# Kernel optimization log

Measured on AMD Instinct MI355X. Metric: run time of the kernel, lower is better.

Reference implementation:

```python
import jax, jax.numpy as jnp
import numpy as np
from jax import lax

M = 8192  # number of candidate detections
C = 80    # number of classes (COCO)
MIN_CONF = 0.25
MIN_IOU = 0.45
VALID_CLASS_IDS = jnp.array([2, 3, 5, 7], dtype=jnp.int32)  # COCO vehicles


def setup_inputs() -> dict:
    key = jax.random.key(0)
    k1, k2, k3, k4, k5, k6, k7 = jax.random.split(key, 7)
    # boxes stored as (y1, x1, y2, x2) in input-image pixel space, guaranteed y1<y2, x1<x2
    y1 = jax.random.uniform(k1, (1, M)) * 600.0
    x1 = jax.random.uniform(k2, (1, M)) * 600.0
    h = jax.random.uniform(k3, (1, M)) * 120.0 + 4.0
    w = jax.random.uniform(k4, (1, M)) * 120.0 + 4.0
    boxes_raw = jnp.stack([y1, x1, y1 + h, x1 + w], axis=-1).astype(jnp.float32)  # [1,M,4]
    scores = jax.random.uniform(k5, (1, C, M), dtype=jnp.float32)  # [1,C,M]
    cls = jax.random.randint(k6, (1, M), 0, C, dtype=jnp.int32)
    idx = jax.random.randint(k7, (1, M), 0, M, dtype=jnp.int32)
    indices = jnp.stack([jnp.zeros_like(cls), cls, idx], axis=-1)  # [1,M,3]: (batch, class_id, box_idx)
    return {"boxes_raw": boxes_raw, "scores": scores, "indices": indices, "out_h": 640, "out_w": 640}


def _pairwise_iou(b):
    # b: [M,4] (x1,y1,x2,y2)
    x1, y1, x2, y2 = b[:, 0], b[:, 1], b[:, 2], b[:, 3]
    area = jnp.maximum(x2 - x1, 0.0) * jnp.maximum(y2 - y1, 0.0)  # [M]
    ix1 = jnp.maximum(x1[:, None], x1[None, :])
    iy1 = jnp.maximum(y1[:, None], y1[None, :])
    ix2 = jnp.minimum(x2[:, None], x2[None, :])
    iy2 = jnp.minimum(y2[:, None], y2[None, :])
    inter = jnp.maximum(ix2 - ix1, 0.0) * jnp.maximum(iy2 - iy1, 0.0)  # [M,M]
    return inter / (area[:, None] + area[None, :] - inter + 1e-9)


def _postprocess(boxes_raw, scores, indices, out_h, out_w):
    idxs = indices[0, :, 2]       # predicted-positive box indices [M]
    class_ids = indices[0, :, 1]  # class ids [M]
    conf = scores[0, class_ids, idxs]  # irregular gather [M]
    b = boxes_raw[0, idxs]  # [M,4] (y1,x1,y2,x2)
    # swap to (x1,y1,x2,y2) as in the original column permutation
    boxes = jnp.stack([b[:, 1], b[:, 0], b[:, 3], b[:, 2]], axis=-1)
    bounds = jnp.array([out_w, out_h, out_w, out_h], dtype=boxes.dtype)
    boxes = jnp.clip(boxes, 0.0, bounds)  # clip_boxes to output image size
    # confidence filter + class filter (as masks; static shapes)
    valid = (conf > MIN_CONF) & jnp.isin(class_ids, VALID_CLASS_IDS)
    # class-agnostic greedy NMS over valid detections
    s = jnp.where(valid, conf, -1.0)
    order = jnp.argsort(-s)  # descending score
    sb = boxes[order]
    sv = valid[order]
    iou = _pairwise_iou(sb)  # [M,M]
    rng = jnp.arange(M)

    def body(i, keep):
        suppress = keep[i] & (iou[i] > MIN_IOU) & (rng > i)
        return keep & ~suppress

    keep_sorted = lax.fori_loop(0, M, body, sv)
    keep = jnp.zeros((M,), dtype=bool).at[order].set(keep_sorted)
    boxes_out = boxes * keep[:, None].astype(boxes.dtype)
    conf_out = conf * keep.astype(conf.dtype)
    return boxes_out, conf_out, class_ids.astype(jnp.int64), keep


def reference(boxes_raw, scores, indices, out_h, out_w):
    return _postprocess(boxes_raw, scores, indices, out_h, out_w)
```

## Files before the change

kernel.cpp:

```cpp
#include <hip/hip_runtime.h>
#include <stdint.h>

#define M_BOXES 8192
#define MIN_CONF_F 0.25f
#define MIN_IOU_F 0.45f
#define VCAP 640
#define NW 10

typedef unsigned long long u64;
typedef unsigned int u32;

#define WS_V      8
#define WS_WCNT   64
#define WS_VKEYS  1024
#define WS_SKEY   66560
#define WS_SBOX   71680
#define WS_SAREA  81920
#define WS_SUP    84480
#define WS_NEED   135680

__device__ inline float scalar_to_float(const int* p) {
    int v = p[0];
    if (v > 0 && v < (1 << 20)) return (float)v;
    return __int_as_float(v);
}

__device__ inline u64 rl64(u64 v, int b) {
    u32 lo = (u32)__builtin_amdgcn_readlane((int)(u32)v, b);
    u32 hi = (u32)__builtin_amdgcn_readlane((int)(u32)(v >> 32), b);
    return ((u64)hi << 32) | lo;
}

__device__ inline u64 wave_or64(u64 v) {
    #pragma unroll
    for (int o = 32; o > 0; o >>= 1) {
        int lo = __shfl_xor((int)(u32)v, o, 64);
        int hi = __shfl_xor((int)(u32)(v >> 32), o, 64);
        v |= ((u64)(u32)hi << 32) | (u32)lo;
    }
    return v;
}

__global__ __launch_bounds__(512) void kA_gather(
    const float* __restrict__ scores, const int* __restrict__ indices,
    float* __restrict__ out, u64* __restrict__ vkeys, int* __restrict__ wcnt)
{
    int tid = threadIdx.x;
    int i = blockIdx.x * 512 + tid;
    int cls = indices[3 * i + 1];
    int idx = indices[3 * i + 2];
    float conf = scores[cls * M_BOXES + idx];
    *reinterpret_cast<float4*>(out + 4 * i) = make_float4(0.f, 0.f, 0.f, 0.f);
    out[4 * M_BOXES + i] = 0.f;
    out[5 * M_BOXES + i] = (float)cls;
    out[6 * M_BOXES + i] = 0.f;
    bool valid = (conf > MIN_CONF_F) &&
                 (cls == 2 || cls == 3 || cls == 5 || cls == 7);
    u64 mask = __ballot(valid);
    int lane = tid & 63;
    int wid = i >> 6;
    if (valid) {
        int pos = (int)__popcll(mask & ((1ull << lane) - 1ull));
        u64 key = ((u64)(~__float_as_uint(conf)) << 32)
                | ((u64)(u32)i << 13) | (u64)(u32)idx;
        vkeys[(wid << 6) + pos] = key;
    }
    if (lane == 0) wcnt[wid] = (int)__popcll(mask);
}

__global__ __launch_bounds__(512) void kS_sort(
    const float* __restrict__ boxes_raw, const int* __restrict__ p_out_h,
    const int* __restrict__ p_out_w, const u64* __restrict__ vkeys,
    const int* __restrict__ wcnt, int* __restrict__ pV,
    u64* __restrict__ skey, float4* __restrict__ sbox,
    float* __restrict__ sarea)
{
    __shared__ int pre_s[129];
    __shared__ u64 tkey[VCAP];
    int tid = threadIdx.x;

    if (tid < 64) {
        int cA = wcnt[tid], cB = wcnt[64 + tid];
        int sA = cA, sB = cB;
        #pragma unroll
        for (int o = 1; o < 64; o <<= 1) {
            int t = __shfl_up(sA, o, 64); if (tid >= o) sA += t;
            int u = __shfl_up(sB, o, 64); if (tid >= o) sB += u;
        }
        int totA = __shfl(sA, 63, 64);
        int totB = __shfl(sB, 63, 64);
        pre_s[tid] = sA - cA;
        pre_s[64 + tid] = totA + sB - cB;
        if (tid == 0) pre_s[128] = totA + totB;
    }
    __syncthreads();
    int V = pre_s[128];
    if (V > VCAP) V = VCAP;
    if (tid == 0) *pV = V;
    if (V <= 0) return;

    for (int s = tid; s < V; s += 512) {
        int lo = 0, hi = 128;
        #pragma unroll
        for (int st = 0; st < 7; ++st) {
            int mid = (lo + hi) >> 1;
            if (pre_s[mid] <= s) lo = mid; else hi = mid;
        }
        tkey[s] = vkeys[(lo << 6) + (s - pre_s[lo])];
    }
    __syncthreads();

    float W = scalar_to_float(p_out_w);
    float H = scalar_to_float(p_out_h);
    for (int s = tid; s < V; s += 512) {
        u64 k = tkey[s];
        int r = 0;
        #pragma unroll 4
        for (int j = 0; j < V; ++j) r += (tkey[j] < k) ? 1 : 0;
        int bidx = (int)(k & 0x1FFFull);
        float4 b = *reinterpret_cast<const float4*>(boxes_raw + 4 * bidx);
        float4 c4;
        c4.x = fminf(fmaxf(b.y, 0.f), W);
        c4.y = fminf(fmaxf(b.x, 0.f), H);
        c4.z = fminf(fmaxf(b.w, 0.f), W);
        c4.w = fminf(fmaxf(b.z, 0.f), H);
        skey[r] = k;
        sbox[r] = c4;
        sarea[r] = fmaxf(c4.z - c4.x, 0.f) * fmaxf(c4.w - c4.y, 0.f);
    }
}

__global__ __launch_bounds__(512) void kM_matrix(
    const float4* __restrict__ sbox, const float* __restrict__ sarea,
    const int* __restrict__ pV, u64* __restrict__ sup)
{
    int V = *pV;
    int nw = (V + 63) >> 6;
    int wave = (blockIdx.x * 512 + threadIdx.x) >> 6;
    int lane = threadIdx.x & 63;
    int bi = wave / NW;
    int w = wave - bi * NW;
    int i0 = bi << 3;
    if (i0 >= V || w >= nw) return;
    int j = (w << 6) + lane;
    bool jv = j < V;
    float4 bj = jv ? sbox[j] : make_float4(0.f, 0.f, 0.f, 0.f);
    float aj = jv ? sarea[j] : 0.f;
    int rend = V - i0; if (rend > 8) rend = 8;
    for (int r = 0; r < rend; ++r) {
        int i = i0 + r;
        float4 bi4 = sbox[i];
        float ai = sarea[i];
        bool p = false;
        if (jv && j > i) {
            float ix1 = fmaxf(bi4.x, bj.x);
            float iy1 = fmaxf(bi4.y, bj.y);
            float ix2 = fminf(bi4.z, bj.z);
            float iy2 = fminf(bi4.w, bj.w);
            float inter = fmaxf(ix2 - ix1, 0.f) * fmaxf(iy2 - iy1, 0.f);
            float iou = inter / (ai + aj - inter + 1e-9f);
            p = iou > MIN_IOU_F;
        }
        u64 bits = __ballot(p);
        if (lane == 0) sup[i * NW + w] = bits;
    }
}

__global__ __launch_bounds__(64) void kZ_scan_scatter(
    float* __restrict__ out, const u64* __restrict__ skey,
    const float4* __restrict__ sbox, const int* __restrict__ pV,
    const u64* __restrict__ supG)
{
    int lane = threadIdx.x;
    int V = *pV;
    if (V <= 0) return;
    int nw = (V + 63) >> 6;

    u64 live[NW], supp[NW];
    #pragma unroll
    for (int w = 0; w < NW; ++w) {
        int c = V - (w << 6);
        live[w] = (c >= 64) ? ~0ull : (c > 0 ? ((1ull << c) - 1ull) : 0ull);
        supp[w] = 0ull;
    }

    u64 rowA[NW], rowB[NW];
    {
        bool rv = lane < V;
        #pragma unroll
        for (int w = 0; w < NW; ++w)
            rowA[w] = (rv && w < nw) ? supG[lane * NW + w] : 0ull;
    }

    auto step = [&](u64 (&rc)[NW], u64 (&rn)[NW], int ci) {
        int rI = ((ci + 1) << 6) + lane;
        bool rv = (ci + 1) < nw && rI < V;
        #pragma unroll
        for (int w = 0; w < NW; ++w)
            rn[w] = (rv && w >= ci + 1 && w < nw) ? supG[rI * NW + w] : 0ull;
        u64 rw = 0, cur = 0;
        #pragma unroll
        for (int w = 0; w < NW; ++w)
            if (w == ci) { rw = rc[w]; cur = live[w] & ~supp[w]; }
        #pragma unroll
        for (int b = 0; b < 64; ++b) {
            u64 rb = rl64(rw, b);
            u64 nxt = cur & ~rb;
            cur = ((cur >> b) & 1ull) ? nxt : cur;
        }
        #pragma unroll
        for (int w = 0; w < NW; ++w) if (w == ci) live[w] = cur;
        #pragma unroll
        for (int w2 = 0; w2 < NW; ++w2)
            if (w2 > ci && w2 < nw) {
                u64 mine = ((cur >> lane) & 1ull) ? rc[w2] : 0ull;
                supp[w2] |= wave_or64(mine);
            }
    };

    int ci = 0;
    while (ci < nw) {
        step(rowA, rowB, ci); ++ci;
        if (ci < nw) { step(rowB, rowA, ci); ++ci; }
    }

    #pragma unroll
    for (int ii = 0; ii < NW; ++ii) {
        int s = (ii << 6) + lane;
        if ((ii << 6) < V && s < V && ((live[ii] >> lane) & 1ull)) {
            u64 k = skey[s];
            u32 orig = (u32)((k >> 13) & 0x1FFFull);
            float conf = __uint_as_float(~(u32)(k >> 32));
            float4 b = sbox[s];
            *reinterpret_cast<float4*>(out + 4 * orig) = b;
            out[4 * M_BOXES + orig] = conf;
            out[6 * M_BOXES + orig] = 1.0f;
        }
    }
}

__global__ __launch_bounds__(256) void fb_gather(
    const float* __restrict__ boxes_raw, const float* __restrict__ scores,
    const int* __restrict__ indices, const int* __restrict__ p_out_h,
    const int* __restrict__ p_out_w, float* __restrict__ out,
    u64* __restrict__ vkeys, float4* __restrict__ vboxes,
    int* __restrict__ vcount)
{
    int i = blockIdx.x * blockDim.x + threadIdx.x;
    if (i >= M_BOXES) return;
    int cls = indices[3 * i + 1];
    int idx = indices[3 * i + 2];
    float conf = scores[cls * M_BOXES + idx];
    *reinterpret_cast<float4*>(out + 4 * i) = make_float4(0.f, 0.f, 0.f, 0.f);
    out[4 * M_BOXES + i] = 0.f;
    out[5 * M_BOXES + i] = (float)cls;
    out[6 * M_BOXES + i] = 0.f;
    bool valid = (conf > MIN_CONF_F) &&
                 (cls == 2 || cls == 3 || cls == 5 || cls == 7);
    if (valid) {
        float4 b = *reinterpret_cast<const float4*>(boxes_raw + 4 * idx);
        float W = scalar_to_float(p_out_w);
        float H = scalar_to_float(p_out_h);
        float4 c;
        c.x = fminf(fmaxf(b.y, 0.f), W);
        c.y = fminf(fmaxf(b.x, 0.f), H);
        c.z = fminf(fmaxf(b.w, 0.f), W);
        c.w = fminf(fmaxf(b.z, 0.f), H);
        int p = atomicAdd(vcount, 1);
        if (p < VCAP) {
            vkeys[p] = ((u64)(~__float_as_uint(conf)) << 32) | (u32)i;
            vboxes[p] = c;
        }
    }
}

__global__ __launch_bounds__(1024) void fb_nms(
    float* __restrict__ out, const u64* __restrict__ vkeys,
    const float4* __restrict__ vboxes, const int* __restrict__ vcount)
{
    __shared__ u64 tkey[VCAP];
    __shared__ u64 skey[VCAP];
    __shared__ float4 sbox[VCAP];
    __shared__ unsigned char keepb[VCAP];
    int tid = threadIdx.x;
    int V = *vcount;
    if (V > VCAP) V = VCAP;
    if (V <= 0) return;
    for (int s = tid; s < V; s += 1024) tkey[s] = vkeys[s];
    __syncthreads();
    for (int s = tid; s < V; s += 1024) {
        u64 k = tkey[s];
        int r = 0;
        for (int j = 0; j < V; ++j) r += (tkey[j] < k);
        skey[r] = k;
        sbox[r] = vboxes[s];
    }
    __syncthreads();
    for (int s = tid; s < V; s += 1024) keepb[s] = 1;
    __syncthreads();
    for (int i = 0; i < V; ++i) {
        if (keepb[i]) {
            float4 bi = sbox[i];
            float ai = fmaxf(bi.z - bi.x, 0.f) * fmaxf(bi.w - bi.y, 0.f);
            for (int s = i + 1 + tid; s < V; s += 1024) {
                if (keepb[s]) {
                    float4 bj = sbox[s];
                    float aj = fmaxf(bj.z - bj.x, 0.f) * fmaxf(bj.w - bj.y, 0.f);
                    float ix1 = fmaxf(bi.x, bj.x);
                    float iy1 = fmaxf(bi.y, bj.y);
                    float ix2 = fminf(bi.z, bj.z);
                    float iy2 = fminf(bi.w, bj.w);
                    float inter = fmaxf(ix2 - ix1, 0.f) * fmaxf(iy2 - iy1, 0.f);
                    float iou = inter / (ai + aj - inter + 1e-9f);
                    if (iou > MIN_IOU_F) keepb[s] = 0;
                }
            }
        }
        __syncthreads();
    }
    for (int s = tid; s < V; s += 1024) {
        if (keepb[s]) {
            u64 k = skey[s];
            u32 orig = (u32)(k & 0xFFFFFFFFull);
            float conf = __uint_as_float(~(u32)(k >> 32));
            float4 b = sbox[s];
            *reinterpret_cast<float4*>(out + 4 * orig) = b;
            out[4 * M_BOXES + orig] = conf;
            out[6 * M_BOXES + orig] = 1.0f;
        }
    }
}

extern "C" void kernel_launch(void* const* d_in, const int* in_sizes, int n_in,
                              void* d_out, int out_size, void* d_ws, size_t ws_size,
                              hipStream_t stream) {
    const float* boxes_raw = (const float*)d_in[0];
    const float* scores    = (const float*)d_in[1];
    const int*   indices   = (const int*)d_in[2];
    const int*   p_out_h   = (const int*)d_in[3];
    const int*   p_out_w   = (const int*)d_in[4];
    float* out = (float*)d_out;
    char* ws = (char*)d_ws;

    if (ws_size >= WS_NEED) {
        int*    pV    = (int*)(ws + WS_V);
        int*    wcnt  = (int*)(ws + WS_WCNT);
        u64*    vkeys = (u64*)(ws + WS_VKEYS);
        u64*    skey  = (u64*)(ws + WS_SKEY);
        float4* sbox  = (float4*)(ws + WS_SBOX);
        float*  sarea = (float*)(ws + WS_SAREA);
        u64*    sup   = (u64*)(ws + WS_SUP);

        kA_gather<<<M_BOXES / 512, 512, 0, stream>>>(
            scores, indices, out, vkeys, wcnt);
        kS_sort<<<1, 512, 0, stream>>>(
            boxes_raw, p_out_h, p_out_w, vkeys, wcnt, pV, skey, sbox, sarea);
        kM_matrix<<<(VCAP / 8) * NW / 8, 512, 0, stream>>>(
            sbox, sarea, pV, sup);
        kZ_scan_scatter<<<1, 64, 0, stream>>>(out, skey, sbox, pV, sup);
    } else {
        int*    vcount = (int*)ws;
        u64*    vkeys  = (u64*)(ws + 16);
        float4* vboxes = (float4*)(ws + 16 + VCAP * sizeof(u64));
        hipMemsetAsync(d_ws, 0, 16, stream);
        fb_gather<<<M_BOXES / 256, 256, 0, stream>>>(
            boxes_raw, scores, indices, p_out_h, p_out_w, out,
            vkeys, vboxes, vcount);
        fb_nms<<<1, 1024, 0, stream>>>(out, vkeys, vboxes, vcount);
    }
}
```

Before: 38.58 us.

## Fuse sort, IoU matrix and NMS scan into one persistent kernel with grid barriers

Replaces the three launches after the gather (single-block rank sort, IoU bitmask matrix, single-wave greedy scan/scatter) with one 16-block kernel that uses atomic-counter grid barriers between phases. The rank sort is now spread across 16 blocks, with each wave computing one key's rank cooperatively through a shuffle reduction instead of one thread looping over all keys. The final scatter uses all 512 threads, reading the live mask from shared memory. This removes two kernel-launch gaps and the serial sort. In exchange it relies on all 16 blocks being co-resident and on correct memory ordering across the global barriers, and it has fewer blocks for the matrix phase.

```diff
diff --git a/kernel.cpp b/kernel.cpp
--- a/kernel.cpp
+++ b/kernel.cpp
@@ -6,11 +6,12 @@
 #define MIN_IOU_F 0.45f
 #define VCAP 640
 #define NW 10
+#define NBLK 16
 
 typedef unsigned long long u64;
 typedef unsigned int u32;
 
-#define WS_V      8
+#define WS_CNT    0
 #define WS_WCNT   64
 #define WS_VKEYS  1024
 #define WS_SKEY   66560
@@ -41,12 +42,24 @@
     return v;
 }
 
+__device__ inline void grid_bar(int* c, int nblk) {
+    __syncthreads();
+    if (threadIdx.x == 0) {
+        __hip_atomic_fetch_add(c, 1, __ATOMIC_ACQ_REL, __HIP_MEMORY_SCOPE_AGENT);
+        while (__hip_atomic_load(c, __ATOMIC_ACQUIRE, __HIP_MEMORY_SCOPE_AGENT) < nblk)
+            __builtin_amdgcn_s_sleep(1);
+    }
+    __syncthreads();
+}
+
 __global__ __launch_bounds__(512) void kA_gather(
     const float* __restrict__ scores, const int* __restrict__ indices,
-    float* __restrict__ out, u64* __restrict__ vkeys, int* __restrict__ wcnt)
+    float* __restrict__ out, u64* __restrict__ vkeys, int* __restrict__ wcnt,
+    int* __restrict__ cnt)
 {
     int tid = threadIdx.x;
     int i = blockIdx.x * 512 + tid;
+    if (i == 0) { cnt[0] = 0; cnt[1] = 0; }
     int cls = indices[3 * i + 1];
     int idx = indices[3 * i + 2];
     float conf = scores[cls * M_BOXES + idx];
@@ -68,16 +81,18 @@
     if (lane == 0) wcnt[wid] = (int)__popcll(mask);
 }
 
-__global__ __launch_bounds__(512) void kS_sort(
+__global__ __launch_bounds__(512) void kMEGA(
     const float* __restrict__ boxes_raw, const int* __restrict__ p_out_h,
-    const int* __restrict__ p_out_w, const u64* __restrict__ vkeys,
-    const int* __restrict__ wcnt, int* __restrict__ pV,
+    const int* __restrict__ p_out_w, float* __restrict__ out,
+    const u64* __restrict__ vkeys, const int* __restrict__ wcnt,
     u64* __restrict__ skey, float4* __restrict__ sbox,
-    float* __restrict__ sarea)
+    float* __restrict__ sarea, u64* __restrict__ sup, int* __restrict__ cnt)
 {
     __shared__ int pre_s[129];
     __shared__ u64 tkey[VCAP];
+    __shared__ u64 live_s[NW];
     int tid = threadIdx.x;
+    int widx = tid >> 6, lane = tid & 63;
 
     if (tid < 64) {
         int cA = wcnt[tid], cB = wcnt[64 + tid];
@@ -96,138 +111,134 @@
     __syncthreads();
     int V = pre_s[128];
     if (V > VCAP) V = VCAP;
-    if (tid == 0) *pV = V;
-    if (V <= 0) return;
-
+
+    if (V > 0) {
+        for (int s = tid; s < V; s += 512) {
+            int lo = 0, hi = 128;
+            #pragma unroll
+            for (int st = 0; st < 7; ++st) {
+                int mid = (lo + hi) >> 1;
+                if (pre_s[mid] <= s) lo = mid; else hi = mid;
+            }
+            tkey[s] = vkeys[(lo << 6) + (s - pre_s[lo])];
+        }
+        __syncthreads();
+
+        float W = scalar_to_float(p_out_w);
+        float H = scalar_to_float(p_out_h);
+        int spb = (V + NBLK - 1) / NBLK;
+        int s0 = blockIdx.x * spb;
+        int send = s0 + spb; if (send > V) send = V;
+        for (int s = s0 + widx; s < send; s += 8) {
+            u64 k = tkey[s];
+            int r = 0;
+            for (int j = lane; j < V; j += 64) r += (tkey[j] < k) ? 1 : 0;
+            #pragma unroll
+            for (int o = 1; o < 64; o <<= 1) r += __shfl_xor(r, o, 64);
+            if (lane == 0) {
+                int bidx = (int)(k & 0x1FFFull);
+                float4 b = *reinterpret_cast<const float4*>(boxes_raw + 4 * bidx);
+                float4 c4;
+                c4.x = fminf(fmaxf(b.y, 0.f), W);
+                c4.y = fminf(fmaxf(b.x, 0.f), H);
+                c4.z = fminf(fmaxf(b.w, 0.f), W);
+                c4.w = fminf(fmaxf(b.z, 0.f), H);
+                skey[r] = k;
+                sbox[r] = c4;
+                sarea[r] = fmaxf(c4.z - c4.x, 0.f) * fmaxf(c4.w - c4.y, 0.f);
+            }
+        }
+    }
+    grid_bar(&cnt[0], NBLK);
+
+    if (V > 0) {
+        int nw = (V + 63) >> 6;
+        int nbi = (V + 7) >> 3;
+        int ntask = nbi * nw;
+        int gwave = blockIdx.x * 8 + widx;
+        for (int t = gwave; t < ntask; t += NBLK * 8) {
+            int bi = t / nw;
+            int w = t - bi * nw;
+            int i0 = bi << 3;
+            int j = (w << 6) + lane;
+            bool jv = j < V;
+            float4 bj = jv ? sbox[j] : make_float4(0.f, 0.f, 0.f, 0.f);
+            float aj = jv ? sarea[j] : 0.f;
+            int rend = V - i0; if (rend > 8) rend = 8;
+            for (int r = 0; r < rend; ++r) {
+                int i = i0 + r;
+                float4 bi4 = sbox[i];
+                float ai = sarea[i];
+                bool p = false;
+                if (jv && j > i) {
+                    float ix1 = fmaxf(bi4.x, bj.x);
+                    float iy1 = fmaxf(bi4.y, bj.y);
+                    float ix2 = fminf(bi4.z, bj.z);
+                    float iy2 = fminf(bi4.w, bj.w);
+                    float inter = fmaxf(ix2 - ix1, 0.f) * fmaxf(iy2 - iy1, 0.f);
+                    float iou = inter / (ai + aj - inter + 1e-9f);
+                    p = iou > MIN_IOU_F;
+                }
+                u64 bits = __ballot(p);
+                if (lane == 0) sup[i * NW + w] = bits;
+            }
+        }
+    }
+    grid_bar(&cnt[1], NBLK);
+
+    if (blockIdx.x != 0 || V <= 0) return;
+    int nw = (V + 63) >> 6;
+    if (tid < 64) {
+        u64 live[NW], supp[NW];
+        #pragma unroll
+        for (int w = 0; w < NW; ++w) {
+            int c = V - (w << 6);
+            live[w] = (c >= 64) ? ~0ull : (c > 0 ? ((1ull << c) - 1ull) : 0ull);
+            supp[w] = 0ull;
+        }
+        u64 rowA[NW], rowB[NW];
+        {
+            bool rv = lane < V;
+            #pragma unroll
+            for (int w = 0; w < NW; ++w)
+                rowA[w] = (rv && w < nw) ? sup[lane * NW + w] : 0ull;
+        }
+        auto step = [&](u64 (&rc)[NW], u64 (&rn)[NW], int ci) {
+            int rI = ((ci + 1) << 6) + lane;
+            bool rv = (ci + 1) < nw && rI < V;
+            #pragma unroll
+            for (int w = 0; w < NW; ++w)
+                rn[w] = (rv && w >= ci + 1 && w < nw) ? sup[rI * NW + w] : 0ull;
+            u64 rw = 0, cur = 0;
+            #pragma unroll
+            for (int w = 0; w < NW; ++w)
+                if (w == ci) { rw = rc[w]; cur = live[w] & ~supp[w]; }
+            #pragma unroll
+            for (int b = 0; b < 64; ++b) {
+                u64 rb = rl64(rw, b);
+                u64 nxt = cur & ~rb;
+                cur = ((cur >> b) & 1ull) ? nxt : cur;
+            }
+            #pragma unroll
+            for (int w = 0; w < NW; ++w) if (w == ci) live[w] = cur;
+            #pragma unroll
+            for (int w2 = 0; w2 < NW; ++w2)
+                if (w2 > ci && w2 < nw) {
+                    u64 mine = ((cur >> lane) & 1ull) ? rc[w2] : 0ull;
+                    supp[w2] |= wave_or64(mine);
+                }
+        };
+        int ci = 0;
+        while (ci < nw) {
+            step(rowA, rowB, ci); ++ci;
+            if (ci < nw) { step(rowB, rowA, ci); ++ci; }
+        }
+        #pragma unroll
+        for (int w = 0; w < NW; ++w) live_s[w] = live[w];
+    }
+    __syncthreads();
     for (int s = tid; s < V; s += 512) {
-        int lo = 0, hi = 128;
-        #pragma unroll
-        for (int st = 0; st < 7; ++st) {
-            int mid = (lo + hi) >> 1;
-            if (pre_s[mid] <= s) lo = mid; else hi = mid;
-        }
-        tkey[s] = vkeys[(lo << 6) + (s - pre_s[lo])];
-    }
-    __syncthreads();
-
-    float W = scalar_to_float(p_out_w);
-    float H = scalar_to_float(p_out_h);
-    for (int s = tid; s < V; s += 512) {
-        u64 k = tkey[s];
-        int r = 0;
-        #pragma unroll 4
-        for (int j = 0; j < V; ++j) r += (tkey[j] < k) ? 1 : 0;
-        int bidx = (int)(k & 0x1FFFull);
-        float4 b = *reinterpret_cast<const float4*>(boxes_raw + 4 * bidx);
-        float4 c4;
-        c4.x = fminf(fmaxf(b.y, 0.f), W);
-        c4.y = fminf(fmaxf(b.x, 0.f), H);
-        c4.z = fminf(fmaxf(b.w, 0.f), W);
-        c4.w = fminf(fmaxf(b.z, 0.f), H);
-        skey[r] = k;
-        sbox[r] = c4;
-        sarea[r] = fmaxf(c4.z - c4.x, 0.f) * fmaxf(c4.w - c4.y, 0.f);
-    }
-}
-
-__global__ __launch_bounds__(512) void kM_matrix(
-    const float4* __restrict__ sbox, const float* __restrict__ sarea,
-    const int* __restrict__ pV, u64* __restrict__ sup)
-{
-    int V = *pV;
-    int nw = (V + 63) >> 6;
-    int wave = (blockIdx.x * 512 + threadIdx.x) >> 6;
-    int lane = threadIdx.x & 63;
-    int bi = wave / NW;
-    int w = wave - bi * NW;
-    int i0 = bi << 3;
-    if (i0 >= V || w >= nw) return;
-    int j = (w << 6) + lane;
-    bool jv = j < V;
-    float4 bj = jv ? sbox[j] : make_float4(0.f, 0.f, 0.f, 0.f);
-    float aj = jv ? sarea[j] : 0.f;
-    int rend = V - i0; if (rend > 8) rend = 8;
-    for (int r = 0; r < rend; ++r) {
-        int i = i0 + r;
-        float4 bi4 = sbox[i];
-        float ai = sarea[i];
-        bool p = false;
-        if (jv && j > i) {
-            float ix1 = fmaxf(bi4.x, bj.x);
-            float iy1 = fmaxf(bi4.y, bj.y);
-            float ix2 = fminf(bi4.z, bj.z);
-            float iy2 = fminf(bi4.w, bj.w);
-            float inter = fmaxf(ix2 - ix1, 0.f) * fmaxf(iy2 - iy1, 0.f);
-            float iou = inter / (ai + aj - inter + 1e-9f);
-            p = iou > MIN_IOU_F;
-        }
-        u64 bits = __ballot(p);
-        if (lane == 0) sup[i * NW + w] = bits;
-    }
-}
-
-__global__ __launch_bounds__(64) void kZ_scan_scatter(
-    float* __restrict__ out, const u64* __restrict__ skey,
-    const float4* __restrict__ sbox, const int* __restrict__ pV,
-    const u64* __restrict__ supG)
-{
-    int lane = threadIdx.x;
-    int V = *pV;
-    if (V <= 0) return;
-    int nw = (V + 63) >> 6;
-
-    u64 live[NW], supp[NW];
-    #pragma unroll
-    for (int w = 0; w < NW; ++w) {
-        int c = V - (w << 6);
-        live[w] = (c >= 64) ? ~0ull : (c > 0 ? ((1ull << c) - 1ull) : 0ull);
-        supp[w] = 0ull;
-    }
-
-    u64 rowA[NW], rowB[NW];
-    {
-        bool rv = lane < V;
-        #pragma unroll
-        for (int w = 0; w < NW; ++w)
-            rowA[w] = (rv && w < nw) ? supG[lane * NW + w] : 0ull;
-    }
-
-    auto step = [&](u64 (&rc)[NW], u64 (&rn)[NW], int ci) {
-        int rI = ((ci + 1) << 6) + lane;
-        bool rv = (ci + 1) < nw && rI < V;
-        #pragma unroll
-        for (int w = 0; w < NW; ++w)
-            rn[w] = (rv && w >= ci + 1 && w < nw) ? supG[rI * NW + w] : 0ull;
-        u64 rw = 0, cur = 0;
-        #pragma unroll
-        for (int w = 0; w < NW; ++w)
-            if (w == ci) { rw = rc[w]; cur = live[w] & ~supp[w]; }
-        #pragma unroll
-        for (int b = 0; b < 64; ++b) {
-            u64 rb = rl64(rw, b);
-            u64 nxt = cur & ~rb;
-            cur = ((cur >> b) & 1ull) ? nxt : cur;
-        }
-        #pragma unroll
-        for (int w = 0; w < NW; ++w) if (w == ci) live[w] = cur;
-        #pragma unroll
-        for (int w2 = 0; w2 < NW; ++w2)
-            if (w2 > ci && w2 < nw) {
-                u64 mine = ((cur >> lane) & 1ull) ? rc[w2] : 0ull;
-                supp[w2] |= wave_or64(mine);
-            }
-    };
-
-    int ci = 0;
-    while (ci < nw) {
-        step(rowA, rowB, ci); ++ci;
-        if (ci < nw) { step(rowB, rowA, ci); ++ci; }
-    }
-
-    #pragma unroll
-    for (int ii = 0; ii < NW; ++ii) {
-        int s = (ii << 6) + lane;
-        if ((ii << 6) < V && s < V && ((live[ii] >> lane) & 1ull)) {
+        if ((live_s[s >> 6] >> (s & 63)) & 1ull) {
             u64 k = skey[s];
             u32 orig = (u32)((k >> 13) & 0x1FFFull);
             float conf = __uint_as_float(~(u32)(k >> 32));
@@ -343,7 +354,7 @@
     char* ws = (char*)d_ws;
 
     if (ws_size >= WS_NEED) {
-        int*    pV    = (int*)(ws + WS_V);
+        int*    cnt   = (int*)(ws + WS_CNT);
         int*    wcnt  = (int*)(ws + WS_WCNT);
         u64*    vkeys = (u64*)(ws + WS_VKEYS);
         u64*    skey  = (u64*)(ws + WS_SKEY);
@@ -352,12 +363,10 @@
         u64*    sup   = (u64*)(ws + WS_SUP);
 
         kA_gather<<<M_BOXES / 512, 512, 0, stream>>>(
-            scores, indices, out, vkeys, wcnt);
-        kS_sort<<<1, 512, 0, stream>>>(
-            boxes_raw, p_out_h, p_out_w, vkeys, wcnt, pV, skey, sbox, sarea);
-        kM_matrix<<<(VCAP / 8) * NW / 8, 512, 0, stream>>>(
-            sbox, sarea, pV, sup);
-        kZ_scan_scatter<<<1, 64, 0, stream>>>(out, skey, sbox, pV, sup);
+            scores, indices, out, vkeys, wcnt, cnt);
+        kMEGA<<<NBLK, 512, 0, stream>>>(
+            boxes_raw, p_out_h, p_out_w, out, vkeys, wcnt,
+            skey, sbox, sarea, sup, cnt);
     } else {
         int*    vcount = (int*)ws;
         u64*    vkeys  = (u64*)(ws + 16);
```

Result: faster. 37.67 us (-2.4%).
